# Optimization experiments

Measured on AMD Instinct MI355X. Metric: run time of the kernel, lower is better.

Reference implementation:

```python
import jax, jax.numpy as jnp
import numpy as np

B, N, M, NUM_CLASSES = 32, 16384, 128, 81
NUM_LOGITS = 5 + NUM_CLASSES - 6  # pred[:, 6:]
SMALL_OBJ_AREA_THR = 0.01
SMALL_OBJ_WEIGHT = 1.5
NEG = -1e9


def setup_inputs() -> dict:
    key = jax.random.key(0)
    k1, k2, k3, k4 = jax.random.split(key, 4)
    preds = jax.random.uniform(k1, (B, N, 5 + NUM_CLASSES), dtype=jnp.float32)
    coords = jax.random.uniform(k2, (B, M, 4), dtype=jnp.float32)
    cls = jax.random.randint(k3, (B, M), 0, NUM_LOGITS).astype(jnp.float32)
    keep = jax.random.uniform(k4, (B, M)) < 0.6
    cls = jnp.where(keep, cls, -1.0)
    targets = jnp.concatenate([coords, cls[..., None]], axis=-1)
    return {"preds": preds, "targets": targets}


def _smooth_l1(x, y):
    d = x - y
    ad = jnp.abs(d)
    return jnp.where(ad < 1.0, 0.5 * d * d, ad - 0.5)


def _bce(p, t):
    # matches torch F.binary_cross_entropy's log clamp at -100
    lp = jnp.maximum(jnp.log(p), -100.0)
    ln = jnp.maximum(jnp.log1p(-p), -100.0)
    return -(t * lp + (1.0 - t) * ln)


def _per_image(pred, target):
    pred_boxes = pred[:, :4]            # [N,4]
    conf = pred[:, 4]                   # [N]
    logits = pred[:, 6:]                # [N, NUM_LOGITS]
    tb = target[:, :4]                  # [M,4]
    valid = target[:, 4] != -1.0        # [M]

    # pairwise IoU [N, M]
    x1 = jnp.maximum(pred_boxes[:, None, 0], tb[None, :, 0])
    y1 = jnp.maximum(pred_boxes[:, None, 1], tb[None, :, 1])
    x2 = jnp.minimum(pred_boxes[:, None, 2], tb[None, :, 2])
    y2 = jnp.minimum(pred_boxes[:, None, 3], tb[None, :, 3])
    inter = jnp.clip(x2 - x1, 0.0) * jnp.clip(y2 - y1, 0.0)
    area1 = (pred_boxes[:, 2] - pred_boxes[:, 0]) * (pred_boxes[:, 3] - pred_boxes[:, 1])
    area2 = (tb[:, 2] - tb[:, 0]) * (tb[:, 3] - tb[:, 1])
    iou = inter / (area1[:, None] + area2[None, :] - inter + 1e-6)
    iou = jnp.where(valid[None, :], iou, NEG)  # mask padded targets out of the max

    best_iou = iou.max(axis=1)          # [N]
    best_idx = iou.argmax(axis=1)       # [N] (first max, like torch)

    matched = best_iou > 0.4
    matched = jnp.where(matched.any(), matched, best_iou == best_iou.max())
    mf = matched.astype(pred.dtype)
    n_m = mf.sum()
    n_m_safe = jnp.maximum(n_m, 1.0)

    g_tb = tb[best_idx]                 # [N,4] matched target boxes
    areas = (g_tb[:, 2] - g_tb[:, 0]) * (g_tb[:, 3] - g_tb[:, 1])
    w = jnp.where(areas < SMALL_OBJ_AREA_THR, SMALL_OBJ_WEIGHT, 1.0)
    bbox = _smooth_l1(pred_boxes, g_tb) * w[:, None]       # [N,4]
    bbox_loss = (bbox * mf[:, None]).sum() / (n_m_safe * 4.0)

    logp = jax.nn.log_softmax(logits, axis=-1)
    cls_idx = jnp.clip(target[best_idx, 4].astype(jnp.int32), 0, NUM_LOGITS - 1)
    nll = -jnp.take_along_axis(logp, cls_idx[:, None], axis=1)[:, 0]
    cls_loss = (nll * mf).sum() / n_m_safe

    m_conf = (_bce(conf, 1.0) * mf).sum() / n_m_safe
    n_u = jnp.asarray(N, pred.dtype) - n_m
    u_conf = (_bce(conf, 0.0) * (1.0 - mf)).sum() / jnp.maximum(n_u, 1.0)
    conf_loss = jnp.where(n_u > 0, (m_conf + u_conf) / 2.0, m_conf)

    full = bbox_loss * 5.0 + cls_loss * 1.0 + conf_loss * 2.0
    empty = _bce(conf, 0.0).mean()
    return jnp.where(valid.any(), full, empty)


def reference(preds, targets):
    per_image = jax.vmap(_per_image)(preds, targets)  # [B]
    return per_image.mean()
```

## Files before the change

kernel.cpp:

```cpp
#include <hip/hip_runtime.h>
#include <math.h>

namespace {

constexpr int B_ = 32;
constexpr int N_ = 16384;
constexpr int M_ = 128;
constexpr int NLOG_ = 80;
constexpr int ROW_ = 86;
constexpr float NEG_ = -1000000000.0f;
constexpr int TPB = 512;
constexpr int BPI = N_ / TPB;
constexpr int BLOCKS = B_ * BPI;
constexpr int RSTR = 16;
constexpr int NW = TPB / 64;

__device__ inline float sl1(float d) {
  float ad = fabsf(d);
  return (ad < 1.0f) ? 0.5f * d * d : ad - 0.5f;
}

__global__ __launch_bounds__(TPB, 8) void k_main(const float* __restrict__ preds,
                                                 const float* __restrict__ targets,
                                                 float* __restrict__ recs) {
  const int b = blockIdx.x / BPI;
  const int blk = blockIdx.x % BPI;
  const int t = threadIdx.x;
  const int lane = t & 63, wid = t >> 6;

  __shared__ float traw[M_ * 5];
  __shared__ float4 sbox[M_];
  __shared__ float sa2e[M_];
  __shared__ float sw_[M_];
  __shared__ float scl[M_];
  __shared__ int scnt2[2];
  __shared__ float smax[NW];
  __shared__ float wacc[NW][12];

  const float* tg = targets + (size_t)b * M_ * 5;
  float tva = tg[t < M_ * 5 ? t : 0];
  float tvb = (t + TPB < M_ * 5) ? tg[t + TPB] : 0.f;

  const float* pb = preds + (size_t)b * N_ * ROW_;
  const int r0 = blk * TPB + t;
  const float* prow = pb + (size_t)r0 * ROW_;
  float2 h01 = *(const float2*)(prow);
  float2 h23 = *(const float2*)(prow + 2);
  float conf = prow[4];

  if (t < M_ * 5) traw[t] = tva;
  if (t + TPB < M_ * 5) traw[t + TPB] = tvb;
  __syncthreads();

  if (t < M_) {
    float bx1 = traw[t * 5 + 0], by1 = traw[t * 5 + 1];
    float bx2 = traw[t * 5 + 2], by2 = traw[t * 5 + 3];
    float bcl = traw[t * 5 + 4];
    bool tvalid = (bcl != -1.0f);
    unsigned long long ball = __ballot(tvalid);
    if (lane == 0) scnt2[wid] = __popcll(ball);
    int tpos = __popcll(ball & ((1ull << lane) - 1ull));
    __syncthreads();
    (void)tpos;
  }
  __syncthreads();
  const int nv = scnt2[0] + scnt2[1];
  const int nvp = (nv + 3) & ~3;
  if (t < M_) {
    float bx1 = traw[t * 5 + 0], by1 = traw[t * 5 + 1];
    float bx2 = traw[t * 5 + 2], by2 = traw[t * 5 + 3];
    float bcl = traw[t * 5 + 4];
    bool tvalid = (bcl != -1.0f);
    unsigned long long ball = __ballot(tvalid);
    int tpos = __popcll(ball & ((1ull << lane) - 1ull));
    if (tvalid) {
      int pos = tpos + (wid ? scnt2[0] : 0);
      sbox[pos] = make_float4(bx1, by1, bx2, by2);
      float ra = (bx2 - bx1) * (by2 - by1);
      sa2e[pos] = ra + 1e-6f;
      sw_[pos] = (ra < 0.01f) ? 1.5f : 1.0f;
      scl[pos] = bcl;
    }
    if (t >= nv && t < nvp) {
      sbox[t] = make_float4(0.f, 0.f, 0.f, 0.f);
      sa2e[t] = __int_as_float(0x7fc00000);
      sw_[t] = 1.0f;
      scl[t] = 0.f;
    }
  }
  __syncthreads();

  float a1 = (h23.x - h01.x) * (h23.y - h01.y);
  float best = NEG_;
  int bj = 0;
  for (int j = 0; j < nvp; j += 4) {
    float4 tb0 = sbox[j], tb1 = sbox[j + 1], tb2 = sbox[j + 2], tb3 = sbox[j + 3];
    float4 aev = *(const float4*)(&sa2e[j]);
    float4 tb[4] = {tb0, tb1, tb2, tb3};
    float ae[4] = {aev.x, aev.y, aev.z, aev.w};
#pragma unroll
    for (int jj = 0; jj < 4; jj++) {
      float x1 = fmaxf(h01.x, tb[jj].x);
      float y1 = fmaxf(h01.y, tb[jj].y);
      float x2 = fminf(h23.x, tb[jj].z);
      float y2 = fminf(h23.y, tb[jj].w);
      float inter = fmaxf(x2 - x1, 0.f) * fmaxf(y2 - y1, 0.f);
      float u = (a1 + ae[jj]) - inter;
      float iou = inter * __builtin_amdgcn_rcpf(u);
      bool gt = iou > best;
      best = gt ? iou : best;
      bj = gt ? (j + jj) : bj;
    }
  }

  float mx = best;
#pragma unroll
  for (int off = 32; off; off >>= 1) mx = fmaxf(mx, __shfl_xor(mx, off));
  if (lane == 0) smax[wid] = mx;
  __syncthreads();
  float blockmax = smax[0];
#pragma unroll
  for (int w = 1; w < NW; w++) blockmax = fmaxf(blockmax, smax[w]);

  float bce0 = -fmaxf(__logf(1.0f - conf), -100.0f);
  bool mA = (nv > 0) && (best > 0.4f);
  bool mB = (nv > 0) && (best == blockmax);
  float v[11] = {0, 0, 0, 0, 0, 0, 0, 0, 0, 0, 0};
  v[5] = bce0;
  if (mA || mB) {
    float4 gb = sbox[bj];
    float w_ = sw_[bj];
    int ci = (int)scl[bj];
    ci = ci < 0 ? 0 : (ci > NLOG_ - 1 ? NLOG_ - 1 : ci);
    float sb = w_ * (sl1(h01.x - gb.x) + sl1(h01.y - gb.y) +
                     sl1(h23.x - gb.z) + sl1(h23.y - gb.w));
    float bce1 = -fmaxf(__logf(conf), -100.0f);
    const float2* l2 = (const float2*)(prow + 6);
    float se = 0.f;
#pragma unroll 10
    for (int k = 0; k < NLOG_ / 2; k++) {
      float2 lv = l2[k];
      se += __expf(lv.x) + __expf(lv.y);
    }
    float nll = __logf(se) - prow[6 + ci];
    if (mA) { v[0] = 1.f; v[1] = sb; v[2] = nll; v[3] = bce1; v[4] = bce0; }
    if (mB) { v[6] = 1.f; v[7] = sb; v[8] = nll; v[9] = bce1; v[10] = bce0; }
  }

#pragma unroll
  for (int i = 0; i < 11; i++) {
    float x = v[i];
#pragma unroll
    for (int off = 32; off; off >>= 1) x += __shfl_xor(x, off);
    if (lane == 0) wacc[wid][i] = x;
  }
  __syncthreads();
  float* rec = recs + (size_t)blockIdx.x * RSTR;
  if (t < 11) {
    float s = 0.f;
#pragma unroll
    for (int w = 0; w < NW; w++) s += wacc[w][t];
    rec[1 + t] = s;
  }
  if (t == 12) rec[0] = blockmax;
  if (t == 13) rec[12] = (float)nv;
}

__global__ __launch_bounds__(256) void k_final(const float* __restrict__ recs,
                                               float* __restrict__ out) {
  const int t = threadIdx.x;
  const int b = t >> 3, g = t & 7;
  __shared__ float limg[B_];

  const float* rb = recs + (size_t)b * BPI * RSTR;
  float aA[6] = {0, 0, 0, 0, 0, 0};
  float bmax = NEG_;
#pragma unroll
  for (int q = 0; q < BPI / 8; q++) {
    const float* r = rb + (size_t)(g + 8 * q) * RSTR;
    bmax = fmaxf(bmax, r[0]);
#pragma unroll
    for (int i = 0; i < 5; i++) aA[i] += r[1 + i];
    aA[5] += r[6];
  }
#pragma unroll
  for (int off = 1; off < 8; off <<= 1) {
    bmax = fmaxf(bmax, __shfl_xor(bmax, off));
#pragma unroll
    for (int i = 0; i < 6; i++) aA[i] += __shfl_xor(aA[i], off);
  }
  float aB[5] = {0, 0, 0, 0, 0};
#pragma unroll
  for (int q = 0; q < BPI / 8; q++) {
    const float* r = rb + (size_t)(g + 8 * q) * RSTR;
    if (r[0] == bmax) {
#pragma unroll
      for (int i = 0; i < 5; i++) aB[i] += r[7 + i];
    }
  }
#pragma unroll
  for (int off = 1; off < 8; off <<= 1) {
#pragma unroll
    for (int i = 0; i < 5; i++) aB[i] += __shfl_xor(aB[i], off);
  }

  if (g == 0) {
    float nv = rb[12];
    float b0all = aA[5];
    float loss;
    if (nv == 0.f) {
      loss = b0all * (1.0f / (float)N_);
    } else {
      float nm, bbox, nll, bce1, bce0m;
      if (aA[0] > 0.f) {
        nm = aA[0]; bbox = aA[1]; nll = aA[2]; bce1 = aA[3]; bce0m = aA[4];
      } else {
        nm = aB[0]; bbox = aB[1]; nll = aB[2]; bce1 = aB[3]; bce0m = aB[4];
      }
      float nms = fmaxf(nm, 1.0f);
      float bbox_loss = bbox / (nms * 4.0f);
      float cls_loss = nll / nms;
      float m_conf = bce1 / nms;
      float n_u = (float)N_ - nm;
      float u_conf = (b0all - bce0m) / fmaxf(n_u, 1.0f);
      float conf_loss = (n_u > 0.f) ? 0.5f * (m_conf + u_conf) : m_conf;
      loss = 5.0f * bbox_loss + cls_loss + 2.0f * conf_loss;
    }
    limg[b] = loss;
  }
  __syncthreads();
  if (t < 32) {
    float x = limg[t];
#pragma unroll
    for (int off = 1; off < 32; off <<= 1) x += __shfl_xor(x, off);
    if (t == 0) out[0] = x * (1.0f / (float)B_);
  }
}

}

extern "C" void kernel_launch(void* const* d_in, const int* in_sizes, int n_in,
                              void* d_out, int out_size, void* d_ws, size_t ws_size,
                              hipStream_t stream) {
  const float* preds = (const float*)d_in[0];
  const float* targets = (const float*)d_in[1];
  float* recs = (float*)d_ws;

  k_main<<<dim3(BLOCKS), dim3(TPB), 0, stream>>>(preds, targets, recs);
  k_final<<<dim3(1), dim3(256), 0, stream>>>(recs, (float*)d_out);
}
```

Measured before the change: 51.66 us.

## Stage pred rows through LDS with coalesced float4 loads, split final reduction

The main kernel now uses 128-thread blocks that first copy a contiguous 128-row tile of predictions into shared memory with coalesced float4 loads. Each thread then reads its row from LDS, replacing the earlier strided per-thread global loads of 86-float rows. Block indices are swizzled across batches, and target setup is simplified because each of the 128 threads owns one target. The single-block final reduction is split into a per-image kernel with 32 blocks plus a tiny final sum, adding a kernel launch and about 44KB of LDS per block, which limits occupancy.

```diff
diff --git a/kernel.cpp b/kernel.cpp
--- a/kernel.cpp
+++ b/kernel.cpp
@@ -9,9 +9,10 @@
 constexpr int NLOG_ = 80;
 constexpr int ROW_ = 86;
 constexpr float NEG_ = -1000000000.0f;
-constexpr int TPB = 512;
-constexpr int BPI = N_ / TPB;
-constexpr int BLOCKS = B_ * BPI;
+constexpr int TILE = 128;
+constexpr int TPB = 128;
+constexpr int TPI = N_ / TILE;
+constexpr int BLOCKS = B_ * TPI;
 constexpr int RSTR = 16;
 constexpr int NW = TPB / 64;
 
@@ -20,90 +21,73 @@
   return (ad < 1.0f) ? 0.5f * d * d : ad - 0.5f;
 }
 
-__global__ __launch_bounds__(TPB, 8) void k_main(const float* __restrict__ preds,
-                                                 const float* __restrict__ targets,
-                                                 float* __restrict__ recs) {
-  const int b = blockIdx.x / BPI;
-  const int blk = blockIdx.x % BPI;
+__global__ __launch_bounds__(TPB) void k_main(const float* __restrict__ preds,
+                                              const float* __restrict__ targets,
+                                              float* __restrict__ recs) {
+  const int gbid = (blockIdx.x & 7) * (BLOCKS / 8) + (blockIdx.x >> 3);
+  const int b = gbid / TPI;
   const int t = threadIdx.x;
   const int lane = t & 63, wid = t >> 6;
 
-  __shared__ float traw[M_ * 5];
+  __shared__ float tile[TILE * ROW_];
   __shared__ float4 sbox[M_];
   __shared__ float sa2e[M_];
   __shared__ float sw_[M_];
   __shared__ float scl[M_];
-  __shared__ int scnt2[2];
+  __shared__ int scnt2[NW];
   __shared__ float smax[NW];
   __shared__ float wacc[NW][12];
 
   const float* tg = targets + (size_t)b * M_ * 5;
-  float tva = tg[t < M_ * 5 ? t : 0];
-  float tvb = (t + TPB < M_ * 5) ? tg[t + TPB] : 0.f;
-
-  const float* pb = preds + (size_t)b * N_ * ROW_;
-  const int r0 = blk * TPB + t;
-  const float* prow = pb + (size_t)r0 * ROW_;
-  float2 h01 = *(const float2*)(prow);
-  float2 h23 = *(const float2*)(prow + 2);
-  float conf = prow[4];
-
-  if (t < M_ * 5) traw[t] = tva;
-  if (t + TPB < M_ * 5) traw[t + TPB] = tvb;
-  __syncthreads();
-
-  if (t < M_) {
-    float bx1 = traw[t * 5 + 0], by1 = traw[t * 5 + 1];
-    float bx2 = traw[t * 5 + 2], by2 = traw[t * 5 + 3];
-    float bcl = traw[t * 5 + 4];
-    bool tvalid = (bcl != -1.0f);
-    unsigned long long ball = __ballot(tvalid);
-    if (lane == 0) scnt2[wid] = __popcll(ball);
-    int tpos = __popcll(ball & ((1ull << lane) - 1ull));
-    __syncthreads();
-    (void)tpos;
-  }
+  float bx1 = tg[t * 5 + 0], by1 = tg[t * 5 + 1];
+  float bx2 = tg[t * 5 + 2], by2 = tg[t * 5 + 3];
+  float bcl = tg[t * 5 + 4];
+
+  {
+    const float4* src4 = (const float4*)(preds + (size_t)gbid * TILE * ROW_);
+    float4* dst4 = (float4*)tile;
+    for (int i = t; i < TILE * ROW_ / 4; i += TPB) dst4[i] = src4[i];
+  }
+
+  bool tvalid = (bcl != -1.0f);
+  unsigned long long ball = __ballot(tvalid);
+  if (lane == 0) scnt2[wid] = __popcll(ball);
+  int tpos = __popcll(ball & ((1ull << lane) - 1ull));
   __syncthreads();
   const int nv = scnt2[0] + scnt2[1];
   const int nvp = (nv + 3) & ~3;
-  if (t < M_) {
-    float bx1 = traw[t * 5 + 0], by1 = traw[t * 5 + 1];
-    float bx2 = traw[t * 5 + 2], by2 = traw[t * 5 + 3];
-    float bcl = traw[t * 5 + 4];
-    bool tvalid = (bcl != -1.0f);
-    unsigned long long ball = __ballot(tvalid);
-    int tpos = __popcll(ball & ((1ull << lane) - 1ull));
-    if (tvalid) {
-      int pos = tpos + (wid ? scnt2[0] : 0);
-      sbox[pos] = make_float4(bx1, by1, bx2, by2);
-      float ra = (bx2 - bx1) * (by2 - by1);
-      sa2e[pos] = ra + 1e-6f;
-      sw_[pos] = (ra < 0.01f) ? 1.5f : 1.0f;
-      scl[pos] = bcl;
-    }
-    if (t >= nv && t < nvp) {
-      sbox[t] = make_float4(0.f, 0.f, 0.f, 0.f);
-      sa2e[t] = __int_as_float(0x7fc00000);
-      sw_[t] = 1.0f;
-      scl[t] = 0.f;
-    }
-  }
-  __syncthreads();
-
-  float a1 = (h23.x - h01.x) * (h23.y - h01.y);
+  if (tvalid) {
+    int pos = tpos + (wid ? scnt2[0] : 0);
+    sbox[pos] = make_float4(bx1, by1, bx2, by2);
+    float ra = (bx2 - bx1) * (by2 - by1);
+    sa2e[pos] = ra + 1e-6f;
+    sw_[pos] = (ra < 0.01f) ? 1.5f : 1.0f;
+    scl[pos] = bcl;
+  }
+  if (t >= nv && t < nvp) {
+    sbox[t] = make_float4(0.f, 0.f, 0.f, 0.f);
+    sa2e[t] = __int_as_float(0x7fc00000);
+    sw_[t] = 1.0f;
+    scl[t] = 0.f;
+  }
+  __syncthreads();
+
+  const float* myrow = &tile[t * ROW_];
+  float px1 = myrow[0], py1 = myrow[1], px2 = myrow[2], py2 = myrow[3];
+  float conf = myrow[4];
+  float a1 = (px2 - px1) * (py2 - py1);
   float best = NEG_;
   int bj = 0;
   for (int j = 0; j < nvp; j += 4) {
-    float4 tb0 = sbox[j], tb1 = sbox[j + 1], tb2 = sbox[j + 2], tb3 = sbox[j + 3];
+    float4 tb[4] = {sbox[j], sbox[j + 1], sbox[j + 2], sbox[j + 3]};
     float4 aev = *(const float4*)(&sa2e[j]);
-    float4 tb[4] = {tb0, tb1, tb2, tb3};
     float ae[4] = {aev.x, aev.y, aev.z, aev.w};
 #pragma unroll
     for (int jj = 0; jj < 4; jj++) {
-      float x1 = fmaxf(h01.x, tb[jj].x);
-      float y1 = fmaxf(h01.y, tb[jj].y);
-      float x2 = fminf(h23.x, tb[jj].z);
-      float y2 = fminf(h23.y, tb[jj].w);
+      float x1 = fmaxf(px1, tb[jj].x);
+      float y1 = fmaxf(py1, tb[jj].y);
+      float x2 = fminf(px2, tb[jj].z);
+      float y2 = fminf(py2, tb[jj].w);
       float inter = fmaxf(x2 - x1, 0.f) * fmaxf(y2 - y1, 0.f);
       float u = (a1 + ae[jj]) - inter;
       float iou = inter * __builtin_amdgcn_rcpf(u);
@@ -118,13 +102,11 @@
   for (int off = 32; off; off >>= 1) mx = fmaxf(mx, __shfl_xor(mx, off));
   if (lane == 0) smax[wid] = mx;
   __syncthreads();
-  float blockmax = smax[0];
-#pragma unroll
-  for (int w = 1; w < NW; w++) blockmax = fmaxf(blockmax, smax[w]);
+  const float tilemax = fmaxf(smax[0], smax[1]);
 
   float bce0 = -fmaxf(__logf(1.0f - conf), -100.0f);
   bool mA = (nv > 0) && (best > 0.4f);
-  bool mB = (nv > 0) && (best == blockmax);
+  bool mB = (nv > 0) && (best == tilemax);
   float v[11] = {0, 0, 0, 0, 0, 0, 0, 0, 0, 0, 0};
   v[5] = bce0;
   if (mA || mB) {
@@ -132,17 +114,17 @@
     float w_ = sw_[bj];
     int ci = (int)scl[bj];
     ci = ci < 0 ? 0 : (ci > NLOG_ - 1 ? NLOG_ - 1 : ci);
-    float sb = w_ * (sl1(h01.x - gb.x) + sl1(h01.y - gb.y) +
-                     sl1(h23.x - gb.z) + sl1(h23.y - gb.w));
+    float sb = w_ * (sl1(px1 - gb.x) + sl1(py1 - gb.y) +
+                     sl1(px2 - gb.z) + sl1(py2 - gb.w));
     float bce1 = -fmaxf(__logf(conf), -100.0f);
-    const float2* l2 = (const float2*)(prow + 6);
+    const float2* l2 = (const float2*)(myrow + 6);
     float se = 0.f;
 #pragma unroll 10
     for (int k = 0; k < NLOG_ / 2; k++) {
       float2 lv = l2[k];
       se += __expf(lv.x) + __expf(lv.y);
     }
-    float nll = __logf(se) - prow[6 + ci];
+    float nll = __logf(se) - myrow[6 + ci];
     if (mA) { v[0] = 1.f; v[1] = sb; v[2] = nll; v[3] = bce1; v[4] = bce0; }
     if (mB) { v[6] = 1.f; v[7] = sb; v[8] = nll; v[9] = bce1; v[10] = bce0; }
   }
@@ -155,67 +137,65 @@
     if (lane == 0) wacc[wid][i] = x;
   }
   __syncthreads();
-  float* rec = recs + (size_t)blockIdx.x * RSTR;
-  if (t < 11) {
-    float s = 0.f;
-#pragma unroll
-    for (int w = 0; w < NW; w++) s += wacc[w][t];
-    rec[1 + t] = s;
-  }
-  if (t == 12) rec[0] = blockmax;
+  float* rec = recs + (size_t)gbid * RSTR;
+  if (t < 11) rec[1 + t] = wacc[0][t] + wacc[1][t];
+  if (t == 12) rec[0] = tilemax;
   if (t == 13) rec[12] = (float)nv;
 }
 
-__global__ __launch_bounds__(256) void k_final(const float* __restrict__ recs,
-                                               float* __restrict__ out) {
-  const int t = threadIdx.x;
-  const int b = t >> 3, g = t & 7;
-  __shared__ float limg[B_];
-
-  const float* rb = recs + (size_t)b * BPI * RSTR;
-  float aA[6] = {0, 0, 0, 0, 0, 0};
-  float bmax = NEG_;
-#pragma unroll
-  for (int q = 0; q < BPI / 8; q++) {
-    const float* r = rb + (size_t)(g + 8 * q) * RSTR;
-    bmax = fmaxf(bmax, r[0]);
-#pragma unroll
-    for (int i = 0; i < 5; i++) aA[i] += r[1 + i];
-    aA[5] += r[6];
-  }
-#pragma unroll
-  for (int off = 1; off < 8; off <<= 1) {
-    bmax = fmaxf(bmax, __shfl_xor(bmax, off));
-#pragma unroll
-    for (int i = 0; i < 6; i++) aA[i] += __shfl_xor(aA[i], off);
-  }
-  float aB[5] = {0, 0, 0, 0, 0};
-#pragma unroll
-  for (int q = 0; q < BPI / 8; q++) {
-    const float* r = rb + (size_t)(g + 8 * q) * RSTR;
-    if (r[0] == bmax) {
-#pragma unroll
-      for (int i = 0; i < 5; i++) aB[i] += r[7 + i];
-    }
-  }
-#pragma unroll
-  for (int off = 1; off < 8; off <<= 1) {
-#pragma unroll
-    for (int i = 0; i < 5; i++) aB[i] += __shfl_xor(aB[i], off);
-  }
-
-  if (g == 0) {
-    float nv = rb[12];
-    float b0all = aA[5];
+__global__ __launch_bounds__(128) void k_fa(const float* __restrict__ recs,
+                                            float* __restrict__ limg) {
+  const int b = blockIdx.x, t = threadIdx.x;
+  const int lane = t & 63, w = t >> 6;
+  __shared__ float sbm[2];
+  __shared__ float sh[2][12];
+
+  const float4* r4 = (const float4*)(recs + ((size_t)b * TPI + t) * RSTR);
+  float4 q0 = r4[0], q1 = r4[1], q2 = r4[2], q3 = r4[3];
+  float rmax = q0.x;
+  float A0 = q0.y, A1 = q0.z, A2 = q0.w, A3 = q1.x, A4 = q1.y, b0 = q1.z;
+  float B0 = q1.w, B1 = q2.x, B2 = q2.y, B3 = q2.z, B4 = q2.w;
+  float nv = q3.x;
+
+  float mx = rmax;
+#pragma unroll
+  for (int off = 32; off; off >>= 1) mx = fmaxf(mx, __shfl_xor(mx, off));
+  if (lane == 0) sbm[w] = mx;
+  __syncthreads();
+  const float gmax = fmaxf(sbm[0], sbm[1]);
+
+  bool sel = (rmax == gmax);
+  float s[12] = {A0, A1, A2, A3, A4, b0,
+                 sel ? B0 : 0.f, sel ? B1 : 0.f, sel ? B2 : 0.f,
+                 sel ? B3 : 0.f, sel ? B4 : 0.f, 0.f};
+#pragma unroll
+  for (int i = 0; i < 11; i++) {
+    float x = s[i];
+#pragma unroll
+    for (int off = 32; off; off >>= 1) x += __shfl_xor(x, off);
+    if (lane == 0) sh[w][i] = x;
+  }
+  __syncthreads();
+  if (t == 0) {
+    float nmA = sh[0][0] + sh[1][0];
+    float b0all = sh[0][5] + sh[1][5];
     float loss;
     if (nv == 0.f) {
       loss = b0all * (1.0f / (float)N_);
     } else {
       float nm, bbox, nll, bce1, bce0m;
-      if (aA[0] > 0.f) {
-        nm = aA[0]; bbox = aA[1]; nll = aA[2]; bce1 = aA[3]; bce0m = aA[4];
+      if (nmA > 0.f) {
+        nm = nmA;
+        bbox = sh[0][1] + sh[1][1];
+        nll = sh[0][2] + sh[1][2];
+        bce1 = sh[0][3] + sh[1][3];
+        bce0m = sh[0][4] + sh[1][4];
       } else {
-        nm = aB[0]; bbox = aB[1]; nll = aB[2]; bce1 = aB[3]; bce0m = aB[4];
+        nm = sh[0][6] + sh[1][6];
+        bbox = sh[0][7] + sh[1][7];
+        nll = sh[0][8] + sh[1][8];
+        bce1 = sh[0][9] + sh[1][9];
+        bce0m = sh[0][10] + sh[1][10];
       }
       float nms = fmaxf(nm, 1.0f);
       float bbox_loss = bbox / (nms * 4.0f);
@@ -228,13 +208,14 @@
     }
     limg[b] = loss;
   }
-  __syncthreads();
-  if (t < 32) {
-    float x = limg[t];
-#pragma unroll
-    for (int off = 1; off < 32; off <<= 1) x += __shfl_xor(x, off);
-    if (t == 0) out[0] = x * (1.0f / (float)B_);
-  }
+}
+
+__global__ void k_fb(const float* __restrict__ limg, float* __restrict__ out) {
+  const int t = threadIdx.x;
+  float x = (t < B_) ? limg[t] : 0.f;
+#pragma unroll
+  for (int off = 32; off; off >>= 1) x += __shfl_xor(x, off);
+  if (t == 0) out[0] = x * (1.0f / (float)B_);
 }
 
 }
@@ -244,8 +225,12 @@
                               hipStream_t stream) {
   const float* preds = (const float*)d_in[0];
   const float* targets = (const float*)d_in[1];
-  float* recs = (float*)d_ws;
+
+  char* ws = (char*)d_ws;
+  float* recs = (float*)ws;
+  float* limg = (float*)(ws + 256 * 1024);
 
   k_main<<<dim3(BLOCKS), dim3(TPB), 0, stream>>>(preds, targets, recs);
-  k_final<<<dim3(1), dim3(256), 0, stream>>>(recs, (float*)d_out);
-}
+  k_fa<<<dim3(B_), dim3(128), 0, stream>>>(recs, limg);
+  k_fb<<<dim3(1), dim3(64), 0, stream>>>(limg, (float*)d_out);
+}
```

After: 103.4 us. 2x slower.

## Fuse final reduction into main kernel via last-block atomic and stage box headers

Applied to the files above, without the earlier changes.

Halves the block size to 256 rows and stages each tile's leading five columns into shared memory with coalesced float4 loads, replacing strided per-row loads. Block indices are swizzled across XCDs. The separate final-reduction kernel is removed: the last block to finish, detected with an atomic ticket counter, runs the per-image and global reduction, saving one launch. The counter is never reset, so it relies on wraparound modulo the block count, and the staging adds index arithmetic and shared-memory traffic.

```diff
diff --git a/kernel.cpp b/kernel.cpp
--- a/kernel.cpp
+++ b/kernel.cpp
@@ -9,11 +9,14 @@
 constexpr int NLOG_ = 80;
 constexpr int ROW_ = 86;
 constexpr float NEG_ = -1000000000.0f;
-constexpr int TPB = 512;
-constexpr int BPI = N_ / TPB;
-constexpr int BLOCKS = B_ * BPI;
+constexpr int TPB = 256;
+constexpr int TILE = 256;
+constexpr int TPI = N_ / TILE;
+constexpr int BLOCKS = B_ * TPI;
 constexpr int RSTR = 16;
 constexpr int NW = TPB / 64;
+constexpr int F4PT = TILE * ROW_ / 4;
+constexpr int SH = 8;
 
 __device__ inline float sl1(float d) {
   float ad = fabsf(d);
@@ -22,12 +25,15 @@
 
 __global__ __launch_bounds__(TPB, 8) void k_main(const float* __restrict__ preds,
                                                  const float* __restrict__ targets,
-                                                 float* __restrict__ recs) {
-  const int b = blockIdx.x / BPI;
-  const int blk = blockIdx.x % BPI;
+                                                 float* __restrict__ recs,
+                                                 unsigned* __restrict__ counter,
+                                                 float* __restrict__ out) {
+  const int gbid = (blockIdx.x & 7) * (BLOCKS / 8) + (blockIdx.x >> 3);
+  const int b = gbid / TPI;
   const int t = threadIdx.x;
   const int lane = t & 63, wid = t >> 6;
 
+  __shared__ float shdr[TILE * SH];
   __shared__ float traw[M_ * 5];
   __shared__ float4 sbox[M_];
   __shared__ float sa2e[M_];
@@ -36,43 +42,53 @@
   __shared__ int scnt2[2];
   __shared__ float smax[NW];
   __shared__ float wacc[NW][12];
+  __shared__ int s_last;
+  __shared__ float limg[B_];
 
   const float* tg = targets + (size_t)b * M_ * 5;
-  float tva = tg[t < M_ * 5 ? t : 0];
-  float tvb = (t + TPB < M_ * 5) ? tg[t + TPB] : 0.f;
-
-  const float* pb = preds + (size_t)b * N_ * ROW_;
-  const int r0 = blk * TPB + t;
-  const float* prow = pb + (size_t)r0 * ROW_;
-  float2 h01 = *(const float2*)(prow);
-  float2 h23 = *(const float2*)(prow + 2);
-  float conf = prow[4];
-
-  if (t < M_ * 5) traw[t] = tva;
-  if (t + TPB < M_ * 5) traw[t + TPB] = tvb;
-  __syncthreads();
-
+  float tva = tg[t];
+  float tvb = tg[t + 256];
+  float tvc = (t < 128) ? tg[t + 512] : 0.f;
+
+  const float* pt = preds + (size_t)gbid * TILE * ROW_;
+  {
+    const float4* src4 = (const float4*)pt;
+    for (int i = t; i < F4PT; i += TPB) {
+      float4 v = src4[i];
+      unsigned dw0 = (unsigned)i * 4u;
+      unsigned row = dw0 / 86u;
+      unsigned col = dw0 - row * 86u;
+      float vals[4] = {v.x, v.y, v.z, v.w};
+#pragma unroll
+      for (int c = 0; c < 4; c++) {
+        if (col < 5u) shdr[row * SH + col] = vals[c];
+        col++;
+        if (col == 86u) { col = 0u; row++; }
+      }
+    }
+  }
+
+  traw[t] = tva;
+  traw[t + 256] = tvb;
+  if (t < 128) traw[t + 512] = tvc;
+  __syncthreads();
+
+  float bx1 = 0, by1 = 0, bx2 = 0, by2 = 0, bcl = 0;
+  bool tvalid = false;
+  int tpos = 0;
   if (t < M_) {
-    float bx1 = traw[t * 5 + 0], by1 = traw[t * 5 + 1];
-    float bx2 = traw[t * 5 + 2], by2 = traw[t * 5 + 3];
-    float bcl = traw[t * 5 + 4];
-    bool tvalid = (bcl != -1.0f);
+    bx1 = traw[t * 5 + 0]; by1 = traw[t * 5 + 1];
+    bx2 = traw[t * 5 + 2]; by2 = traw[t * 5 + 3];
+    bcl = traw[t * 5 + 4];
+    tvalid = (bcl != -1.0f);
     unsigned long long ball = __ballot(tvalid);
     if (lane == 0) scnt2[wid] = __popcll(ball);
-    int tpos = __popcll(ball & ((1ull << lane) - 1ull));
-    __syncthreads();
-    (void)tpos;
+    tpos = __popcll(ball & ((1ull << lane) - 1ull));
   }
   __syncthreads();
   const int nv = scnt2[0] + scnt2[1];
   const int nvp = (nv + 3) & ~3;
   if (t < M_) {
-    float bx1 = traw[t * 5 + 0], by1 = traw[t * 5 + 1];
-    float bx2 = traw[t * 5 + 2], by2 = traw[t * 5 + 3];
-    float bcl = traw[t * 5 + 4];
-    bool tvalid = (bcl != -1.0f);
-    unsigned long long ball = __ballot(tvalid);
-    int tpos = __popcll(ball & ((1ull << lane) - 1ull));
     if (tvalid) {
       int pos = tpos + (wid ? scnt2[0] : 0);
       sbox[pos] = make_float4(bx1, by1, bx2, by2);
@@ -90,20 +106,22 @@
   }
   __syncthreads();
 
-  float a1 = (h23.x - h01.x) * (h23.y - h01.y);
+  float4 hb = *(const float4*)(&shdr[t * SH]);
+  float conf = shdr[t * SH + 4];
+  float px1 = hb.x, py1 = hb.y, px2 = hb.z, py2 = hb.w;
+  float a1 = (px2 - px1) * (py2 - py1);
   float best = NEG_;
   int bj = 0;
   for (int j = 0; j < nvp; j += 4) {
-    float4 tb0 = sbox[j], tb1 = sbox[j + 1], tb2 = sbox[j + 2], tb3 = sbox[j + 3];
+    float4 tb[4] = {sbox[j], sbox[j + 1], sbox[j + 2], sbox[j + 3]};
     float4 aev = *(const float4*)(&sa2e[j]);
-    float4 tb[4] = {tb0, tb1, tb2, tb3};
     float ae[4] = {aev.x, aev.y, aev.z, aev.w};
 #pragma unroll
     for (int jj = 0; jj < 4; jj++) {
-      float x1 = fmaxf(h01.x, tb[jj].x);
-      float y1 = fmaxf(h01.y, tb[jj].y);
-      float x2 = fminf(h23.x, tb[jj].z);
-      float y2 = fminf(h23.y, tb[jj].w);
+      float x1 = fmaxf(px1, tb[jj].x);
+      float y1 = fmaxf(py1, tb[jj].y);
+      float x2 = fminf(px2, tb[jj].z);
+      float y2 = fminf(py2, tb[jj].w);
       float inter = fmaxf(x2 - x1, 0.f) * fmaxf(y2 - y1, 0.f);
       float u = (a1 + ae[jj]) - inter;
       float iou = inter * __builtin_amdgcn_rcpf(u);
@@ -118,13 +136,11 @@
   for (int off = 32; off; off >>= 1) mx = fmaxf(mx, __shfl_xor(mx, off));
   if (lane == 0) smax[wid] = mx;
   __syncthreads();
-  float blockmax = smax[0];
-#pragma unroll
-  for (int w = 1; w < NW; w++) blockmax = fmaxf(blockmax, smax[w]);
+  const float tilemax = fmaxf(fmaxf(smax[0], smax[1]), fmaxf(smax[2], smax[3]));
 
   float bce0 = -fmaxf(__logf(1.0f - conf), -100.0f);
   bool mA = (nv > 0) && (best > 0.4f);
-  bool mB = (nv > 0) && (best == blockmax);
+  bool mB = (nv > 0) && (best == tilemax);
   float v[11] = {0, 0, 0, 0, 0, 0, 0, 0, 0, 0, 0};
   v[5] = bce0;
   if (mA || mB) {
@@ -132,9 +148,10 @@
     float w_ = sw_[bj];
     int ci = (int)scl[bj];
     ci = ci < 0 ? 0 : (ci > NLOG_ - 1 ? NLOG_ - 1 : ci);
-    float sb = w_ * (sl1(h01.x - gb.x) + sl1(h01.y - gb.y) +
-                     sl1(h23.x - gb.z) + sl1(h23.y - gb.w));
+    float sb = w_ * (sl1(px1 - gb.x) + sl1(py1 - gb.y) +
+                     sl1(px2 - gb.z) + sl1(py2 - gb.w));
     float bce1 = -fmaxf(__logf(conf), -100.0f);
+    const float* prow = pt + (size_t)t * ROW_;
     const float2* l2 = (const float2*)(prow + 6);
     float se = 0.f;
 #pragma unroll 10
@@ -155,78 +172,78 @@
     if (lane == 0) wacc[wid][i] = x;
   }
   __syncthreads();
-  float* rec = recs + (size_t)blockIdx.x * RSTR;
-  if (t < 11) {
-    float s = 0.f;
-#pragma unroll
-    for (int w = 0; w < NW; w++) s += wacc[w][t];
-    rec[1 + t] = s;
-  }
-  if (t == 12) rec[0] = blockmax;
+  float* rec = recs + (size_t)gbid * RSTR;
+  if (t < 11) rec[1 + t] = wacc[0][t] + wacc[1][t] + wacc[2][t] + wacc[3][t];
+  if (t == 12) rec[0] = tilemax;
   if (t == 13) rec[12] = (float)nv;
-}
-
-__global__ __launch_bounds__(256) void k_final(const float* __restrict__ recs,
-                                               float* __restrict__ out) {
-  const int t = threadIdx.x;
-  const int b = t >> 3, g = t & 7;
-  __shared__ float limg[B_];
-
-  const float* rb = recs + (size_t)b * BPI * RSTR;
-  float aA[6] = {0, 0, 0, 0, 0, 0};
-  float bmax = NEG_;
-#pragma unroll
-  for (int q = 0; q < BPI / 8; q++) {
-    const float* r = rb + (size_t)(g + 8 * q) * RSTR;
-    bmax = fmaxf(bmax, r[0]);
-#pragma unroll
-    for (int i = 0; i < 5; i++) aA[i] += r[1 + i];
-    aA[5] += r[6];
-  }
-#pragma unroll
-  for (int off = 1; off < 8; off <<= 1) {
-    bmax = fmaxf(bmax, __shfl_xor(bmax, off));
-#pragma unroll
-    for (int i = 0; i < 6; i++) aA[i] += __shfl_xor(aA[i], off);
-  }
-  float aB[5] = {0, 0, 0, 0, 0};
-#pragma unroll
-  for (int q = 0; q < BPI / 8; q++) {
-    const float* r = rb + (size_t)(g + 8 * q) * RSTR;
-    if (r[0] == bmax) {
-#pragma unroll
-      for (int i = 0; i < 5; i++) aB[i] += r[7 + i];
-    }
-  }
-#pragma unroll
-  for (int off = 1; off < 8; off <<= 1) {
-#pragma unroll
-    for (int i = 0; i < 5; i++) aB[i] += __shfl_xor(aB[i], off);
-  }
-
-  if (g == 0) {
-    float nv = rb[12];
-    float b0all = aA[5];
-    float loss;
-    if (nv == 0.f) {
-      loss = b0all * (1.0f / (float)N_);
-    } else {
-      float nm, bbox, nll, bce1, bce0m;
-      if (aA[0] > 0.f) {
-        nm = aA[0]; bbox = aA[1]; nll = aA[2]; bce1 = aA[3]; bce0m = aA[4];
+  __syncthreads();
+
+  if (t == 0) {
+    __threadfence();
+    unsigned tk = atomicAdd(counter, 1u);
+    s_last = ((tk & (unsigned)(BLOCKS - 1)) == (unsigned)(BLOCKS - 1)) ? 1 : 0;
+  }
+  __syncthreads();
+  if (!s_last) return;
+  __threadfence();
+
+  {
+    const int im = t >> 3, g = t & 7;
+    const float* rb = recs + (size_t)im * TPI * RSTR;
+    float aA[6] = {0, 0, 0, 0, 0, 0};
+    float bmax = NEG_;
+#pragma unroll
+    for (int q = 0; q < TPI / 8; q++) {
+      const float* r = rb + (size_t)(g + 8 * q) * RSTR;
+      bmax = fmaxf(bmax, r[0]);
+#pragma unroll
+      for (int i = 0; i < 5; i++) aA[i] += r[1 + i];
+      aA[5] += r[6];
+    }
+#pragma unroll
+    for (int off = 1; off < 8; off <<= 1) {
+      bmax = fmaxf(bmax, __shfl_xor(bmax, off));
+#pragma unroll
+      for (int i = 0; i < 6; i++) aA[i] += __shfl_xor(aA[i], off);
+    }
+    float aB[5] = {0, 0, 0, 0, 0};
+#pragma unroll
+    for (int q = 0; q < TPI / 8; q++) {
+      const float* r = rb + (size_t)(g + 8 * q) * RSTR;
+      if (r[0] == bmax) {
+#pragma unroll
+        for (int i = 0; i < 5; i++) aB[i] += r[7 + i];
+      }
+    }
+#pragma unroll
+    for (int off = 1; off < 8; off <<= 1) {
+#pragma unroll
+      for (int i = 0; i < 5; i++) aB[i] += __shfl_xor(aB[i], off);
+    }
+    if (g == 0) {
+      float nvf = rb[12];
+      float b0all = aA[5];
+      float loss;
+      if (nvf == 0.f) {
+        loss = b0all * (1.0f / (float)N_);
       } else {
-        nm = aB[0]; bbox = aB[1]; nll = aB[2]; bce1 = aB[3]; bce0m = aB[4];
+        float nm, bbox, nll, bce1, bce0m;
+        if (aA[0] > 0.f) {
+          nm = aA[0]; bbox = aA[1]; nll = aA[2]; bce1 = aA[3]; bce0m = aA[4];
+        } else {
+          nm = aB[0]; bbox = aB[1]; nll = aB[2]; bce1 = aB[3]; bce0m = aB[4];
+        }
+        float nms = fmaxf(nm, 1.0f);
+        float bbox_loss = bbox / (nms * 4.0f);
+        float cls_loss = nll / nms;
+        float m_conf = bce1 / nms;
+        float n_u = (float)N_ - nm;
+        float u_conf = (b0all - bce0m) / fmaxf(n_u, 1.0f);
+        float conf_loss = (n_u > 0.f) ? 0.5f * (m_conf + u_conf) : m_conf;
+        loss = 5.0f * bbox_loss + cls_loss + 2.0f * conf_loss;
       }
-      float nms = fmaxf(nm, 1.0f);
-      float bbox_loss = bbox / (nms * 4.0f);
-      float cls_loss = nll / nms;
-      float m_conf = bce1 / nms;
-      float n_u = (float)N_ - nm;
-      float u_conf = (b0all - bce0m) / fmaxf(n_u, 1.0f);
-      float conf_loss = (n_u > 0.f) ? 0.5f * (m_conf + u_conf) : m_conf;
-      loss = 5.0f * bbox_loss + cls_loss + 2.0f * conf_loss;
-    }
-    limg[b] = loss;
+      limg[im] = loss;
+    }
   }
   __syncthreads();
   if (t < 32) {
@@ -244,8 +261,11 @@
                               hipStream_t stream) {
   const float* preds = (const float*)d_in[0];
   const float* targets = (const float*)d_in[1];
-  float* recs = (float*)d_ws;
-
-  k_main<<<dim3(BLOCKS), dim3(TPB), 0, stream>>>(preds, targets, recs);
-  k_final<<<dim3(1), dim3(256), 0, stream>>>(recs, (float*)d_out);
-}
+
+  char* ws = (char*)d_ws;
+  float* recs = (float*)ws;
+  unsigned* counter = (unsigned*)(ws + 131072);
+
+  k_main<<<dim3(BLOCKS), dim3(TPB), 0, stream>>>(preds, targets, recs, counter,
+                                                 (float*)d_out);
+}
```

Measured after the change: 88.46 us. +71.2%, slower.
